# Performance work log

Hardware: AMD Instinct MI355X
Metric: run time of the kernel (lower is better)

## Reference

```python
import jax, jax.numpy as jnp
import numpy as np

EPS = 1e-05

def _rms_norm(x, w, eps=EPS):
    xf = x.astype(jnp.float32)
    var = jnp.mean(xf * xf, axis=-1, keepdims=True)
    return (x * jax.lax.rsqrt(var + eps)) * w

def _apply_rotary_emb(x, freqs_cis):
    # x: [B,S,H,D], freqs_cis: [B,S,D] with cos in first half, sin in second
    half = freqs_cis.shape[-1] // 2
    cos = freqs_cis[..., :half][:, :, None, :]  # [B,S,1,D/2]
    sin = freqs_cis[..., half:][:, :, None, :]
    xf = x.astype(jnp.float32).reshape(*x.shape[:-1], -1, 2)
    xr, xi = xf[..., 0], xf[..., 1]
    out_r = xr * cos - xi * sin
    out_i = xr * sin + xi * cos
    out = jnp.stack([out_r, out_i], axis=-1).reshape(x.shape)
    return out.astype(x.dtype)

def setup_inputs() -> dict:
    key = jax.random.key(0)
    ks = jax.random.split(key, 8)
    B, S, D, H = 2, 4096, 2048, 16
    hd = D // H
    scale = 1.0 / np.sqrt(D)
    x = jax.random.normal(ks[0], (B, S, D), dtype=jnp.float32)
    freqs_cis = jax.random.normal(ks[1], (B, S, hd), dtype=jnp.float32)
    wq = jax.random.normal(ks[2], (D, D), dtype=jnp.float32) * scale
    wk = jax.random.normal(ks[3], (D, D), dtype=jnp.float32) * scale
    wv = jax.random.normal(ks[4], (D, D), dtype=jnp.float32) * scale
    wo = jax.random.normal(ks[5], (D, D), dtype=jnp.float32) * scale
    norm_q_w = jnp.ones((hd,), dtype=jnp.float32)
    norm_k_w = jnp.ones((hd,), dtype=jnp.float32)
    return {"x": x, "freqs_cis": freqs_cis, "wq": wq, "wk": wk, "wv": wv,
            "wo": wo, "norm_q_w": norm_q_w, "norm_k_w": norm_k_w}

def reference(x, freqs_cis, wq, wk, wv, wo, norm_q_w, norm_k_w):
    B, S, D = x.shape
    H = 16
    hd = D // H
    # Linear with torch convention: y = x @ W^T
    q = (x @ wq.T).reshape(B, S, H, hd)
    k = (x @ wk.T).reshape(B, S, H, hd)
    v = (x @ wv.T).reshape(B, S, H, hd)
    q = _rms_norm(q, norm_q_w)
    k = _rms_norm(k, norm_k_w)
    q = _apply_rotary_emb(q, freqs_cis)
    k = _apply_rotary_emb(k, freqs_cis)
    # SDPA: [B,H,S,hd]
    scale = 1.0 / jnp.sqrt(jnp.asarray(hd, dtype=jnp.float32))
    scores = jnp.einsum('bqhd,bkhd->bhqk', q, k) * scale
    attn = jax.nn.softmax(scores, axis=-1)
    out = jnp.einsum('bhqk,bkhd->bqhd', attn, v).reshape(B, S, D)
    return out @ wo.T
```

## Files before the change

kernel.cpp:

```cpp
#include <hip/hip_runtime.h>
#include <hip/hip_bf16.h>
#include <cstdint>
#include <cstdio>

typedef unsigned short ushort_t;
typedef __attribute__((ext_vector_type(8))) __bf16 bf16x8;
typedef __attribute__((ext_vector_type(2))) __bf16 bhalf2_t;
typedef __attribute__((ext_vector_type(8))) unsigned short us8;
typedef __attribute__((ext_vector_type(4))) unsigned short us4;
typedef __attribute__((ext_vector_type(4))) float f32x4;
typedef __attribute__((ext_vector_type(2))) float f32x2;

__device__ __forceinline__ ushort_t f2b(float f) {
  uint32_t u = __builtin_bit_cast(uint32_t, f);
  uint32_t r = (u + 0x7fffu + ((u >> 16) & 1u)) >> 16;
  return (ushort_t)r;
}
__device__ __forceinline__ float b2f(ushort_t s) {
  return __builtin_bit_cast(float, (uint32_t)s << 16);
}

__device__ __forceinline__ void gld_lds16(const void* g, void* l) {
  __builtin_amdgcn_global_load_lds(
      (__attribute__((address_space(1))) void*)(uintptr_t)g,
      (__attribute__((address_space(3))) void*)(uint32_t)(uintptr_t)l,
      16, 0, 0);
}

__global__ void cast_f2b(const float* __restrict__ src, ushort_t* __restrict__ dst, int n4) {
  int i = blockIdx.x * 256 + threadIdx.x;
  if (i < n4) {
    float4 f = ((const float4*)src)[i];
    us4 o = { f2b(f.x), f2b(f.y), f2b(f.z), f2b(f.w) };
    ((us4*)dst)[i] = o;
  }
}

template <typename OutT>
__global__ __launch_bounds__(256, 3) void gemm_bt(const ushort_t* __restrict__ A,
                                                  const ushort_t* __restrict__ B,
                                                  OutT* __restrict__ C,
                                                  int M, int N, int K) {
  __shared__ ushort_t As[128 * 64];
  __shared__ ushort_t Bs[128 * 64];
  const int w    = threadIdx.x >> 6;
  const int lane = threadIdx.x & 63;
  const int m_l  = lane & 15;
  const int quad = lane >> 4;
  const int m0 = blockIdx.y * 128, n0 = blockIdx.x * 128;
  const int wr = (w >> 1) * 64, wc = (w & 1) * 64;

  f32x4 acc[4][4];
#pragma unroll
  for (int i = 0; i < 4; ++i)
#pragma unroll
    for (int j = 0; j < 4; ++j) acc[i][j] = (f32x4){0.f, 0.f, 0.f, 0.f};

  const int lr = lane >> 3;
  const int sc8 = ((lane & 7) ^ lr) * 8;

  for (int k0 = 0; k0 < K; k0 += 64) {
#pragma unroll
    for (int t = 0; t < 4; ++t) {
      int ra = w * 32 + t * 8;
      gld_lds16(A + (size_t)(m0 + ra + lr) * K + k0 + sc8, &As[ra * 64]);
      gld_lds16(B + (size_t)(n0 + ra + lr) * K + k0 + sc8, &Bs[ra * 64]);
    }
    __syncthreads();
#pragma unroll
    for (int kk = 0; kk < 2; ++kk) {
      bf16x8 af[4], bf[4];
#pragma unroll
      for (int mt = 0; mt < 4; ++mt) {
        int row = wr + mt * 16 + m_l;
        af[mt] = __builtin_bit_cast(bf16x8,
            *(const us8*)&As[row * 64 + ((kk * 4 + quad) ^ (m_l & 7)) * 8]);
      }
#pragma unroll
      for (int nt = 0; nt < 4; ++nt) {
        int row = wc + nt * 16 + m_l;
        bf[nt] = __builtin_bit_cast(bf16x8,
            *(const us8*)&Bs[row * 64 + ((kk * 4 + quad) ^ (m_l & 7)) * 8]);
      }
#pragma unroll
      for (int mt = 0; mt < 4; ++mt)
#pragma unroll
        for (int nt = 0; nt < 4; ++nt)
          acc[mt][nt] = __builtin_amdgcn_mfma_f32_16x16x32_bf16(af[mt], bf[nt], acc[mt][nt], 0, 0, 0);
    }
    __syncthreads();
  }
#pragma unroll
  for (int mt = 0; mt < 4; ++mt)
#pragma unroll
    for (int nt = 0; nt < 4; ++nt)
#pragma unroll
      for (int r = 0; r < 4; ++r) {
        int row = m0 + wr + mt * 16 + quad * 4 + r;
        int col = n0 + wc + nt * 16 + m_l;
        float v = acc[mt][nt][r];
        if constexpr (__is_same(OutT, float)) C[(size_t)row * N + col] = v;
        else                                  C[(size_t)row * N + col] = f2b(v);
      }
}

__global__ void rmsrope(ushort_t* __restrict__ qkv, const float* __restrict__ freqs,
                        const float* __restrict__ wq, const float* __restrict__ wk) {
  int w = threadIdx.x >> 6, lane = threadIdx.x & 63;
  int rid = blockIdx.x * 4 + w;
  int h = rid & 15;
  int m = (rid >> 4) & 8191;
  int qk = rid >> 17;
  ushort_t* row = qkv + (size_t)m * 6144 + qk * 2048 + h * 128;
  uint32_t pr = *(const uint32_t*)(row + 2 * lane);
  float xr = b2f((ushort_t)(pr & 0xffff));
  float xi = b2f((ushort_t)(pr >> 16));
  float ss = xr * xr + xi * xi;
#pragma unroll
  for (int o = 1; o < 64; o <<= 1) ss += __shfl_xor(ss, o);
  float rinv = rsqrtf(ss * (1.f / 128.f) + 1e-5f);
  const float* wn = qk ? wk : wq;
  float nr = xr * rinv * wn[2 * lane];
  float ni = xi * rinv * wn[2 * lane + 1];
  float fc = freqs[(size_t)m * 128 + lane];
  float fs = freqs[(size_t)m * 128 + 64 + lane];
  float orr = nr * fc - ni * fs;
  float oii = nr * fs + ni * fc;
  const float k1 = 0.08838834764831845f * 1.4426950408889634f;
  float fscale = (qk == 0) ? k1 : 1.0f;
  orr *= fscale;
  oii *= fscale;
  *(uint32_t*)(row + 2 * lane) = (uint32_t)f2b(orr) | ((uint32_t)f2b(oii) << 16);
}

__global__ void transpose_v(const ushort_t* __restrict__ qkv, ushort_t* __restrict__ vt) {
  __shared__ ushort_t tile[64][136];
  int bh = blockIdx.y, s0 = blockIdx.x * 64;
  int b = bh >> 4, h = bh & 15;
  const ushort_t* src = qkv + (size_t)(b * 4096 + s0) * 6144 + 4096 + h * 128;
  int t = threadIdx.x;
  int r = t >> 2, c0 = (t & 3) * 32;
#pragma unroll
  for (int j = 0; j < 4; ++j)
    *(us8*)&tile[r][c0 + 8 * j] = *(const us8*)(src + (size_t)r * 6144 + c0 + 8 * j);
  __syncthreads();
  int d = t >> 1, sh = (t & 1) * 32;
  ushort_t* dst = vt + (size_t)bh * 524288 + (size_t)d * 4096 + s0 + sh;
#pragma unroll
  for (int i0 = 0; i0 < 32; i0 += 8) {
    us8 o;
#pragma unroll
    for (int j = 0; j < 8; ++j) o[j] = tile[sh + i0 + j][d];
    *(us8*)(dst + i0) = o;
  }
}

__global__ __launch_bounds__(256, 5) void flash_attn(const ushort_t* __restrict__ qkv,
                                                     const ushort_t* __restrict__ vt,
                                                     ushort_t* __restrict__ ctx) {
  __shared__ ushort_t Ks[64 * 128];
  __shared__ ushort_t VTs[128 * 64];

  const int w = threadIdx.x >> 6, lane = threadIdx.x & 63;
  const int m_l = lane & 15, quad = lane >> 4;
  const int bh = blockIdx.y, b = bh >> 4, h = bh & 15;
  const int q0 = blockIdx.x * 64;

  const ushort_t* qb = qkv + (size_t)(b * 4096 + q0) * 6144 + h * 128;
  const ushort_t* kb = qkv + (size_t)(b * 4096) * 6144 + 2048 + h * 128;
  const ushort_t* vb = vt + (size_t)bh * 524288;

  const int lr = lane >> 4, p15 = lane & 15;

  {
#pragma unroll
    for (int t = 0; t < 4; ++t) {
      int rbase = w * 16 + t * 4;
      int sst = lr | ((t >> 1) << 2) | ((w & 1) << 3);
      gld_lds16(qb + (size_t)(rbase + lr) * 6144 + (p15 ^ sst) * 8, &Ks[rbase * 128]);
    }
  }
  __syncthreads();
  bf16x8 qf[4];
  {
    int rowq = w * 16 + m_l;
    int sqr = (m_l & 3) | ((m_l >> 3) << 2) | ((w & 1) << 3);
#pragma unroll
    for (int kk = 0; kk < 4; ++kk)
      qf[kk] = __builtin_bit_cast(bf16x8,
          *(const us8*)&Ks[rowq * 128 + ((kk * 4 + quad) ^ sqr) * 8]);
  }

  int kbase[4];
#pragma unroll
  for (int mt = 0; mt < 4; ++mt)
    kbase[mt] = ((m_l >> 2) * 8 + (m_l & 3) + (mt & 1) * 4 + (mt >> 1) * 32) * 128;
  int cx[4];
#pragma unroll
  for (int kk = 0; kk < 4; ++kk) cx[kk] = ((kk * 4 + quad) ^ m_l) * 8;
  int vx[2];
#pragma unroll
  for (int kk = 0; kk < 2; ++kk) vx[kk] = ((kk * 4 + quad) ^ (m_l & 7)) * 8;

  f32x4 lacc = (f32x4){0.f, 0.f, 0.f, 0.f};
  f32x4 Oa[8];
#pragma unroll
  for (int nt = 0; nt < 8; ++nt) Oa[nt] = (f32x4){0.f, 0.f, 0.f, 0.f};

  for (int kv0 = 0; kv0 < 4096; kv0 += 64) {
    __syncthreads();
    {
#pragma unroll
      for (int t = 0; t < 4; ++t) {
        int rbase = w * 16 + t * 4;
        int sst = lr | ((t >> 1) << 2) | ((w & 1) << 3);
        gld_lds16(kb + (size_t)(kv0 + rbase + lr) * 6144 + (p15 ^ sst) * 8, &Ks[rbase * 128]);
      }
      int lr2 = lane >> 3, s2 = (lane & 7) ^ lr2;
#pragma unroll
      for (int t = 0; t < 4; ++t) {
        int r = w * 32 + t * 8;
        gld_lds16(vb + (size_t)(r + lr2) * 4096 + kv0 + s2 * 8, &VTs[r * 64]);
      }
    }
    __syncthreads();

    f32x4 S[4];
#pragma unroll
    for (int mt = 0; mt < 4; ++mt) S[mt] = (f32x4){0.f, 0.f, 0.f, 0.f};
#pragma unroll
    for (int kk = 0; kk < 4; ++kk)
#pragma unroll
      for (int mt = 0; mt < 4; ++mt) {
        bf16x8 kf = __builtin_bit_cast(bf16x8, *(const us8*)&Ks[kbase[mt] + cx[kk]]);
        S[mt] = __builtin_amdgcn_mfma_f32_16x16x32_bf16(kf, qf[kk], S[mt], 0, 0, 0);
      }

    f32x4 pe[4];
#pragma unroll
    for (int mt = 0; mt < 4; ++mt)
#pragma unroll
      for (int r = 0; r < 4; ++r)
        pe[mt][r] = __builtin_amdgcn_exp2f(S[mt][r]);

    lacc += (pe[0] + pe[1]) + (pe[2] + pe[3]);

    union Upf { us8 u; bhalf2_t h[4]; } pf[2];
#pragma unroll
    for (int kk = 0; kk < 2; ++kk)
#pragma unroll
      for (int t = 0; t < 4; ++t) {
        int mt = kk * 2 + (t >> 1), r0 = (t & 1) * 2;
        f32x2 a = { pe[mt][r0], pe[mt][r0 + 1] };
        pf[kk].h[t] = __builtin_convertvector(a, bhalf2_t);
      }

#pragma unroll
    for (int kk = 0; kk < 2; ++kk) {
      bf16x8 pfr = __builtin_bit_cast(bf16x8, pf[kk].u);
#pragma unroll
      for (int nt = 0; nt < 8; ++nt) {
        bf16x8 vf = __builtin_bit_cast(bf16x8,
            *(const us8*)&VTs[(nt * 16 + m_l) * 64 + vx[kk]]);
        Oa[nt] = __builtin_amdgcn_mfma_f32_16x16x32_bf16(pfr, vf, Oa[nt], 0, 0, 0);
      }
    }
  }

  float lsum = (lacc[0] + lacc[1]) + (lacc[2] + lacc[3]);
  lsum += __shfl_xor(lsum, 16);
  lsum += __shfl_xor(lsum, 32);

#pragma unroll
  for (int r = 0; r < 4; ++r) {
    float inv = 1.f / __shfl(lsum, (lane >> 4) * 4 + r);
    int s = q0 + w * 16 + quad * 4 + r;
    ushort_t* dst = ctx + (size_t)(b * 4096 + s) * 2048 + h * 128;
#pragma unroll
    for (int nt = 0; nt < 8; ++nt) dst[nt * 16 + m_l] = f2b(Oa[nt][r] * inv);
  }
}

extern "C" void kernel_launch(void* const* d_in, const int* in_sizes, int n_in,
                              void* d_out, int out_size, void* d_ws, size_t ws_size,
                              hipStream_t stream) {
  const float* x     = (const float*)d_in[0];
  const float* freqs = (const float*)d_in[1];
  const float* wq    = (const float*)d_in[2];
  const float* wk    = (const float*)d_in[3];
  const float* wv    = (const float*)d_in[4];
  const float* wo    = (const float*)d_in[5];
  const float* nqw   = (const float*)d_in[6];
  const float* nkw   = (const float*)d_in[7];
  float* out = (float*)d_out;

  char* ws = (char*)d_ws;
  ushort_t* xb    = (ushort_t*)(ws);
  ushort_t* wqkvb = (ushort_t*)(ws + 33554432);
  ushort_t* wob   = (ushort_t*)(ws + 58720256);
  ushort_t* qkvb  = (ushort_t*)(ws + 67108864);
  ushort_t* vtb   = (ushort_t*)(ws + 167772160);
  ushort_t* ctxb  = (ushort_t*)(ws + 201326592);
  if (ws_size < 234881024) { fprintf(stderr, "kernel_launch: ws too small (%zu < 234881024)\n", ws_size); return; }

  cast_f2b<<<16384, 256, 0, stream>>>(x, xb, 4194304);
  cast_f2b<<<4096, 256, 0, stream>>>(wq, wqkvb, 1048576);
  cast_f2b<<<4096, 256, 0, stream>>>(wk, wqkvb + 2048 * 2048, 1048576);
  cast_f2b<<<4096, 256, 0, stream>>>(wv, wqkvb + 2 * 2048 * 2048, 1048576);
  cast_f2b<<<4096, 256, 0, stream>>>(wo, wob, 1048576);

  gemm_bt<ushort_t><<<dim3(48, 64), 256, 0, stream>>>(xb, wqkvb, qkvb, 8192, 6144, 2048);
  rmsrope<<<65536, 256, 0, stream>>>(qkvb, freqs, nqw, nkw);
  transpose_v<<<dim3(64, 32), 256, 0, stream>>>(qkvb, vtb);
  flash_attn<<<dim3(64, 32), 256, 0, stream>>>(qkvb, vtb, ctxb);
  gemm_bt<float><<<dim3(16, 64), 256, 0, stream>>>(ctxb, wob, out, 8192, 2048, 2048);
}
```

Baseline: 856.3 us.

## Process two query tiles per flash-attention block to reuse K/V tiles

Each flash-attention block now handles 128 query rows by giving each wave two 16-row query groups that share the same K and V tiles loaded into LDS. This halves K/V global loads and LDS reads per query, raising MFMA density per sync. In exchange, accumulator and score registers double, occupancy bound drops from 5 to 3 blocks, and the grid halves, which may cause tail imbalance.

```diff
diff --git a/kernel.cpp b/kernel.cpp
--- a/kernel.cpp
+++ b/kernel.cpp
@@ -155,7 +155,7 @@
   }
 }
 
-__global__ __launch_bounds__(256, 5) void flash_attn(const ushort_t* __restrict__ qkv,
+__global__ __launch_bounds__(256, 3) void flash_attn(const ushort_t* __restrict__ qkv,
                                                      const ushort_t* __restrict__ vt,
                                                      ushort_t* __restrict__ ctx) {
   __shared__ ushort_t Ks[64 * 128];
@@ -164,7 +164,7 @@
   const int w = threadIdx.x >> 6, lane = threadIdx.x & 63;
   const int m_l = lane & 15, quad = lane >> 4;
   const int bh = blockIdx.y, b = bh >> 4, h = bh & 15;
-  const int q0 = blockIdx.x * 64;
+  const int q0 = blockIdx.x * 128;
 
   const ushort_t* qb = qkv + (size_t)(b * 4096 + q0) * 6144 + h * 128;
   const ushort_t* kb = qkv + (size_t)(b * 4096) * 6144 + 2048 + h * 128;
@@ -172,22 +172,22 @@
 
   const int lr = lane >> 4, p15 = lane & 15;
 
-  {
+  bf16x8 qf[2][4];
+  const int rowq = w * 16 + m_l;
+  const int sqr = (m_l & 3) | ((m_l >> 3) << 2) | ((w & 1) << 3);
+#pragma unroll
+  for (int g = 0; g < 2; ++g) {
+    __syncthreads();
 #pragma unroll
     for (int t = 0; t < 4; ++t) {
       int rbase = w * 16 + t * 4;
       int sst = lr | ((t >> 1) << 2) | ((w & 1) << 3);
-      gld_lds16(qb + (size_t)(rbase + lr) * 6144 + (p15 ^ sst) * 8, &Ks[rbase * 128]);
-    }
-  }
-  __syncthreads();
-  bf16x8 qf[4];
-  {
-    int rowq = w * 16 + m_l;
-    int sqr = (m_l & 3) | ((m_l >> 3) << 2) | ((w & 1) << 3);
+      gld_lds16(qb + (size_t)(g * 64 + rbase + lr) * 6144 + (p15 ^ sst) * 8, &Ks[rbase * 128]);
+    }
+    __syncthreads();
 #pragma unroll
     for (int kk = 0; kk < 4; ++kk)
-      qf[kk] = __builtin_bit_cast(bf16x8,
+      qf[g][kk] = __builtin_bit_cast(bf16x8,
           *(const us8*)&Ks[rowq * 128 + ((kk * 4 + quad) ^ sqr) * 8]);
   }
 
@@ -202,10 +202,12 @@
 #pragma unroll
   for (int kk = 0; kk < 2; ++kk) vx[kk] = ((kk * 4 + quad) ^ (m_l & 7)) * 8;
 
-  f32x4 lacc = (f32x4){0.f, 0.f, 0.f, 0.f};
-  f32x4 Oa[8];
-#pragma unroll
-  for (int nt = 0; nt < 8; ++nt) Oa[nt] = (f32x4){0.f, 0.f, 0.f, 0.f};
+  f32x4 lacc[2] = {(f32x4){0.f, 0.f, 0.f, 0.f}, (f32x4){0.f, 0.f, 0.f, 0.f}};
+  f32x4 Oa[2][8];
+#pragma unroll
+  for (int g = 0; g < 2; ++g)
+#pragma unroll
+    for (int nt = 0; nt < 8; ++nt) Oa[g][nt] = (f32x4){0.f, 0.f, 0.f, 0.f};
 
   for (int kv0 = 0; kv0 < 4096; kv0 += 64) {
     __syncthreads();
@@ -225,59 +227,67 @@
     }
     __syncthreads();
 
-    f32x4 S[4];
-#pragma unroll
-    for (int mt = 0; mt < 4; ++mt) S[mt] = (f32x4){0.f, 0.f, 0.f, 0.f};
+    f32x4 S[2][4];
+#pragma unroll
+    for (int g = 0; g < 2; ++g)
+#pragma unroll
+      for (int mt = 0; mt < 4; ++mt) S[g][mt] = (f32x4){0.f, 0.f, 0.f, 0.f};
 #pragma unroll
     for (int kk = 0; kk < 4; ++kk)
 #pragma unroll
       for (int mt = 0; mt < 4; ++mt) {
         bf16x8 kf = __builtin_bit_cast(bf16x8, *(const us8*)&Ks[kbase[mt] + cx[kk]]);
-        S[mt] = __builtin_amdgcn_mfma_f32_16x16x32_bf16(kf, qf[kk], S[mt], 0, 0, 0);
-      }
-
-    f32x4 pe[4];
-#pragma unroll
-    for (int mt = 0; mt < 4; ++mt)
-#pragma unroll
-      for (int r = 0; r < 4; ++r)
-        pe[mt][r] = __builtin_amdgcn_exp2f(S[mt][r]);
-
-    lacc += (pe[0] + pe[1]) + (pe[2] + pe[3]);
-
-    union Upf { us8 u; bhalf2_t h[4]; } pf[2];
-#pragma unroll
-    for (int kk = 0; kk < 2; ++kk)
-#pragma unroll
-      for (int t = 0; t < 4; ++t) {
-        int mt = kk * 2 + (t >> 1), r0 = (t & 1) * 2;
-        f32x2 a = { pe[mt][r0], pe[mt][r0 + 1] };
-        pf[kk].h[t] = __builtin_convertvector(a, bhalf2_t);
-      }
+        S[0][mt] = __builtin_amdgcn_mfma_f32_16x16x32_bf16(kf, qf[0][kk], S[0][mt], 0, 0, 0);
+        S[1][mt] = __builtin_amdgcn_mfma_f32_16x16x32_bf16(kf, qf[1][kk], S[1][mt], 0, 0, 0);
+      }
+
+    union Upf { us8 u; bhalf2_t h[4]; } pf[2][2];
+#pragma unroll
+    for (int g = 0; g < 2; ++g) {
+      f32x4 pe[4];
+#pragma unroll
+      for (int mt = 0; mt < 4; ++mt)
+#pragma unroll
+        for (int r = 0; r < 4; ++r)
+          pe[mt][r] = __builtin_amdgcn_exp2f(S[g][mt][r]);
+      lacc[g] += (pe[0] + pe[1]) + (pe[2] + pe[3]);
+#pragma unroll
+      for (int kk = 0; kk < 2; ++kk)
+#pragma unroll
+        for (int t = 0; t < 4; ++t) {
+          int mt = kk * 2 + (t >> 1), r0 = (t & 1) * 2;
+          f32x2 a = { pe[mt][r0], pe[mt][r0 + 1] };
+          pf[g][kk].h[t] = __builtin_convertvector(a, bhalf2_t);
+        }
+    }
 
 #pragma unroll
     for (int kk = 0; kk < 2; ++kk) {
-      bf16x8 pfr = __builtin_bit_cast(bf16x8, pf[kk].u);
+      bf16x8 p0 = __builtin_bit_cast(bf16x8, pf[0][kk].u);
+      bf16x8 p1 = __builtin_bit_cast(bf16x8, pf[1][kk].u);
 #pragma unroll
       for (int nt = 0; nt < 8; ++nt) {
         bf16x8 vf = __builtin_bit_cast(bf16x8,
             *(const us8*)&VTs[(nt * 16 + m_l) * 64 + vx[kk]]);
-        Oa[nt] = __builtin_amdgcn_mfma_f32_16x16x32_bf16(pfr, vf, Oa[nt], 0, 0, 0);
-      }
-    }
-  }
-
-  float lsum = (lacc[0] + lacc[1]) + (lacc[2] + lacc[3]);
-  lsum += __shfl_xor(lsum, 16);
-  lsum += __shfl_xor(lsum, 32);
-
-#pragma unroll
-  for (int r = 0; r < 4; ++r) {
-    float inv = 1.f / __shfl(lsum, (lane >> 4) * 4 + r);
-    int s = q0 + w * 16 + quad * 4 + r;
-    ushort_t* dst = ctx + (size_t)(b * 4096 + s) * 2048 + h * 128;
-#pragma unroll
-    for (int nt = 0; nt < 8; ++nt) dst[nt * 16 + m_l] = f2b(Oa[nt][r] * inv);
+        Oa[0][nt] = __builtin_amdgcn_mfma_f32_16x16x32_bf16(p0, vf, Oa[0][nt], 0, 0, 0);
+        Oa[1][nt] = __builtin_amdgcn_mfma_f32_16x16x32_bf16(p1, vf, Oa[1][nt], 0, 0, 0);
+      }
+    }
+  }
+
+#pragma unroll
+  for (int g = 0; g < 2; ++g) {
+    float lsum = (lacc[g][0] + lacc[g][1]) + (lacc[g][2] + lacc[g][3]);
+    lsum += __shfl_xor(lsum, 16);
+    lsum += __shfl_xor(lsum, 32);
+#pragma unroll
+    for (int r = 0; r < 4; ++r) {
+      float inv = 1.f / __shfl(lsum, quad * 4 + r);
+      int s = q0 + g * 64 + w * 16 + quad * 4 + r;
+      ushort_t* dst = ctx + (size_t)(b * 4096 + s) * 2048 + h * 128;
+#pragma unroll
+      for (int nt = 0; nt < 8; ++nt) dst[nt * 16 + m_l] = f2b(Oa[g][nt][r] * inv);
+    }
   }
 }
 
@@ -312,6 +322,6 @@
   gemm_bt<ushort_t><<<dim3(48, 64), 256, 0, stream>>>(xb, wqkvb, qkvb, 8192, 6144, 2048);
   rmsrope<<<65536, 256, 0, stream>>>(qkvb, freqs, nqw, nkw);
   transpose_v<<<dim3(64, 32), 256, 0, stream>>>(qkvb, vtb);
-  flash_attn<<<dim3(64, 32), 256, 0, stream>>>(qkvb, vtb, ctxb);
+  flash_attn<<<dim3(32, 32), 256, 0, stream>>>(qkvb, vtb, ctxb);
   gemm_bt<float><<<dim3(16, 64), 256, 0, stream>>>(ctxb, wob, out, 8192, 2048, 2048);
 }
```

Result: no change. 845.8 us (-1.2%).
